# Kernel optimization log

Measured on AMD Instinct MI355X. Metric: run time of the kernel, lower is better.

The kernel has to match this reference:

```python
import jax, jax.numpy as jnp
import numpy as np
import math

N_HEADS = 16
DIM = 1024

def setup_inputs() -> dict:
    key = jax.random.key(0)
    ks = jax.random.split(key, 10)
    B, S, D = 4, 2048, DIM
    xavier = math.sqrt(2.0 / (D + D))  # xavier_normal_ std for square weight
    query = jax.random.normal(ks[0], (B, S, D), dtype=jnp.float32)
    mask = jnp.ones((B, S), dtype=jnp.int32)
    Wq = jax.random.normal(ks[1], (D, D), dtype=jnp.float32) * xavier
    Wk = jax.random.normal(ks[2], (D, D), dtype=jnp.float32) * xavier
    Wv = jax.random.normal(ks[3], (D, D), dtype=jnp.float32) * xavier
    Wo = jax.random.normal(ks[4], (D, D), dtype=jnp.float32) * xavier
    bound = 1.0 / math.sqrt(D)  # default nn.Linear bias init U(-1/sqrt(fan_in), ...)
    bq = jax.random.uniform(ks[5], (D,), jnp.float32, -bound, bound)
    bk = jax.random.uniform(ks[6], (D,), jnp.float32, -bound, bound)
    bv = jax.random.uniform(ks[7], (D,), jnp.float32, -bound, bound)
    bo = jax.random.uniform(ks[8], (D,), jnp.float32, -bound, bound)
    return {"query": query, "mask": mask, "Wq": Wq, "bq": bq, "Wk": Wk, "bk": bk,
            "Wv": Wv, "bv": bv, "Wo": Wo, "bo": bo}

def reference(query, mask, Wq, bq, Wk, bk, Wv, bv, Wo, bo):
    B, S, D = query.shape
    H = N_HEADS
    Dh = D // H
    scale = math.sqrt(Dh)
    def heads(x):  # [B,S,D] -> [B,H,S,Dh]
        return x.reshape(B, S, H, Dh).transpose(0, 2, 1, 3)
    q = heads(query @ Wq.T + bq)
    k = heads(query @ Wk.T + bk)
    v = heads(query @ Wv.T + bv)
    scores = jnp.einsum('bhsd,bhtd->bhst', q, k)  # [B,H,S,S]
    keep = (mask != 0)[:, None, None, :]  # [B,1,1,S]
    scores = jnp.where(keep, scores, jnp.float32(-1e20))
    attn = jax.nn.softmax(scores / scale, axis=-1)
    ctx = jnp.einsum('bhst,bhtd->bhsd', attn, v)  # [B,H,S,Dh]
    ctx = ctx.transpose(0, 2, 1, 3).reshape(B, S, D)
    return ctx @ Wo.T + bo
```

## Files before the change

kernel.cpp:

```cpp
#include <hip/hip_runtime.h>

typedef unsigned short u16;
typedef unsigned int u32;
typedef __attribute__((ext_vector_type(8))) short short8;
typedef __attribute__((ext_vector_type(8))) __bf16 bf16x8;
typedef __attribute__((ext_vector_type(4))) float f32x4;
typedef __attribute__((ext_vector_type(2))) u32 u32x2;

__device__ __forceinline__ float bf2f(u16 u) { return __uint_as_float(((u32)u) << 16); }
__device__ __forceinline__ u16 f2bf(float f) {
  u32 u = __float_as_uint(f);
  u = (u + 0x7fffu + ((u >> 16) & 1u)) >> 16;
  return (u16)u;
}

__device__ __forceinline__ float EXP2(float x) {
#if __has_builtin(__builtin_amdgcn_exp2f)
  return __builtin_amdgcn_exp2f(x);
#else
  return exp2f(x);
#endif
}

__device__ __forceinline__ u32 CVTPK(float lo, float hi) {
  u32 r;
  asm("v_cvt_pk_bf16_f32 %0, %1, %2" : "=v"(r) : "v"(lo), "v"(hi));
  return r;
}

template <typename V>
__device__ __forceinline__ auto mfma_try(V a, V b, f32x4 c, int)
    -> decltype(__builtin_amdgcn_mfma_f32_16x16x32_bf16(a, b, c, 0, 0, 0)) {
  return __builtin_amdgcn_mfma_f32_16x16x32_bf16(a, b, c, 0, 0, 0);
}
template <typename V>
__device__ __forceinline__ f32x4 mfma_try(V a, V b, f32x4 c, long) {
  return __builtin_amdgcn_mfma_f32_16x16x32_bf16(
      __builtin_bit_cast(bf16x8, a), __builtin_bit_cast(bf16x8, b), c, 0, 0, 0);
}
__device__ __forceinline__ f32x4 MFMA(short8 a, short8 b, f32x4 c) {
  return mfma_try(a, b, c, 0);
}

#define GLOAD16(gsrc, ldst)                                                  \
  __builtin_amdgcn_global_load_lds(                                          \
      (const __attribute__((address_space(1))) void*)(gsrc),                 \
      (__attribute__((address_space(3))) void*)(ldst), 16, 0, 0)

#define SQ 2048
#define NH 16
#define DH 64
#define DMODEL 1024

__global__ void detect_dtype(const u16* __restrict__ q, int* __restrict__ flag) {
  __shared__ int cnt;
  if (threadIdx.x == 0) cnt = 0;
  __syncthreads();
  const int k = threadIdx.x * 16384 + 128;
  const u16 u = q[2 * k];
  const int e = (u >> 7) & 0xFF;
  if (e >= 96 && e <= 143) atomicAdd(&cnt, 1);
  __syncthreads();
  if (threadIdx.x == 0) *flag = (cnt < 128) ? 1 : 0;
}

__device__ __forceinline__ short8 cvt8_f32(const float* s) {
  f32x4 a = *(const f32x4*)s;
  f32x4 b = *(const f32x4*)(s + 4);
  short8 o;
#pragma unroll
  for (int j = 0; j < 4; ++j) o[j] = (short)f2bf(a[j]);
#pragma unroll
  for (int j = 0; j < 4; ++j) o[4 + j] = (short)f2bf(b[j]);
  return o;
}

__global__ void cvt_tensor(const void* __restrict__ src, u16* __restrict__ dst,
                           int n8, const int* __restrict__ flag) {
  const bool isf32 = (*flag != 0);
  int i = blockIdx.x * blockDim.x + threadIdx.x;
  const int stride = gridDim.x * blockDim.x;
  if (isf32) {
    const float* s = (const float*)src;
    for (; i < n8; i += stride) *(short8*)(dst + i * 8) = cvt8_f32(s + i * 8);
  } else {
    const short8* s = (const short8*)src;
    for (; i < n8; i += stride) *(short8*)(dst + i * 8) = s[i];
  }
}

__global__ void cvt_w4(const void* s0, const void* s1, const void* s2, const void* s3,
                       u16* __restrict__ dst, const int* __restrict__ flag) {
  const bool isf32 = (*flag != 0);
  int i = blockIdx.x * blockDim.x + threadIdx.x;
  const int stride = gridDim.x * blockDim.x;
  for (; i < (1 << 19); i += stride) {
    const int seg = i >> 17, off = i & ((1 << 17) - 1);
    const void* s = (seg == 0) ? s0 : (seg == 1) ? s1 : (seg == 2) ? s2 : s3;
    u16* d = dst + ((long)seg << 20) + (long)off * 8;
    if (isf32) *(short8*)d = cvt8_f32((const float*)s + off * 8);
    else *(short8*)d = *((const short8*)s + off);
  }
}

__global__ void cvt_b4(const void* s0, const void* s1, const void* s2, const void* s3,
                       u16* __restrict__ dst, const int* __restrict__ flag) {
  const bool isf32 = (*flag != 0);
  int i = blockIdx.x * blockDim.x + threadIdx.x;
  if (i >= 512) return;
  const int seg = i >> 7, off = i & 127;
  const void* s = (seg == 0) ? s0 : (seg == 1) ? s1 : (seg == 2) ? s2 : s3;
  u16* d = dst + seg * 1024 + off * 8;
  if (isf32) *(short8*)d = cvt8_f32((const float*)s + off * 8);
  else *(short8*)d = *((const short8*)s + off);
}

template <int MODE>
__global__ __launch_bounds__(256, 2) void gemm_bt(
    const u16* __restrict__ A, const u16* __restrict__ W,
    const u16* __restrict__ bias, void* __restrict__ Cv,
    const int* __restrict__ flag, int M, int N, int K) {
  __shared__ __align__(16) u16 As[128 * 32];
  __shared__ __align__(16) u16 Bs[128 * 32];
  const int tid = threadIdx.x;
  const int lane = tid & 63;
  const int wv = tid >> 6;
  const int wr = wv >> 1, wc = wv & 1;
  const bool isf32 = (MODE == 0) && (*flag != 0);

  const int nwg = gridDim.x;
  const int cpx = nwg >> 3;
  const int bid = (blockIdx.x % 8) * cpx + (blockIdx.x >> 3);

  const int tiles_n = N >> 7;
  const int tm = bid / tiles_n, tn = bid % tiles_n;
  const int m0 = tm << 7, n0 = tn << 7;

  f32x4 acc[4][4];
#pragma unroll
  for (int i = 0; i < 4; ++i)
#pragma unroll
    for (int j = 0; j < 4; ++j)
#pragma unroll
      for (int r = 0; r < 4; ++r) acc[i][j][r] = 0.f;

  const int srow = tid >> 2;
  const int skk = (tid & 3) * 8;
  const u16* a0 = A + (long)(m0 + srow) * K + skk;
  const u16* a1 = A + (long)(m0 + 64 + srow) * K + skk;
  const u16* b0 = W + (long)(n0 + srow) * K + skk;
  const u16* b1 = W + (long)(n0 + 64 + srow) * K + skk;
  u16* lA0 = &As[tid * 8];
  u16* lA1 = &As[(256 + tid) * 8];
  u16* lB0 = &Bs[tid * 8];
  u16* lB1 = &Bs[(256 + tid) * 8];

  const int rk = 8 * (lane >> 4);
  const int rrow = lane & 15;
  const int r0 = (lane >> 4) * 4;

  for (int k0 = 0; k0 < K; k0 += 32) {
    GLOAD16(a0 + k0, lA0);
    GLOAD16(a1 + k0, lA1);
    GLOAD16(b0 + k0, lB0);
    GLOAD16(b1 + k0, lB1);
    asm volatile("s_waitcnt vmcnt(0)" ::: "memory");
    __syncthreads();
    short8 af[4], bf[4];
#pragma unroll
    for (int mi = 0; mi < 4; ++mi)
      af[mi] = *(const short8*)&As[(wr * 64 + mi * 16 + rrow) * 32 + rk];
#pragma unroll
    for (int ni = 0; ni < 4; ++ni)
      bf[ni] = *(const short8*)&Bs[(wc * 64 + ni * 16 + rrow) * 32 + rk];
#pragma unroll
    for (int mi = 0; mi < 4; ++mi)
#pragma unroll
      for (int ni = 0; ni < 4; ++ni)
        acc[mi][ni] = MFMA(af[mi], bf[ni], acc[mi][ni]);
    __syncthreads();
  }

#pragma unroll
  for (int ni = 0; ni < 4; ++ni) {
    const int col = n0 + wc * 64 + ni * 16 + rrow;
    const float bv = bf2f(bias[col]);
#pragma unroll
    for (int mi = 0; mi < 4; ++mi) {
#pragma unroll
      for (int r = 0; r < 4; ++r) {
        const int row = m0 + wr * 64 + mi * 16 + r0 + r;
        const float v = acc[mi][ni][r] + bv;
        if (MODE == 0) {
          const long idx = (long)row * N + col;
          if (isf32) ((float*)Cv)[idx] = v;
          else ((u16*)Cv)[idx] = f2bf(v);
        } else if (MODE == 1) {
          const int b = row >> 11, s = row & 2047, h = col >> 6, dh = col & 63;
          ((u16*)Cv)[(((long)(b * NH + h) * SQ) + s) * DH + dh] = f2bf(v);
        } else {
          const int b = row >> 11, s = row & 2047, h = col >> 6, dh = col & 63;
          ((u16*)Cv)[(((long)(b * NH + h) * DH) + dh) * SQ + s] = f2bf(v);
        }
      }
    }
  }
}

#define LSTR 72
#define SM_C 0.18033688011112043f

__global__ __launch_bounds__(256, 2) void attn_kernel(
    const u16* __restrict__ q, const u16* __restrict__ k,
    const u16* __restrict__ vT, const int* __restrict__ mask,
    u16* __restrict__ ctx) {
  __shared__ __align__(16) u16 Ks[64 * LSTR];
  __shared__ __align__(16) u16 Vs[64 * LSTR];
  __shared__ __align__(16) u16 Ps[4][32 * LSTR];
  __shared__ __align__(16) float Msf[64];

  const int tid = threadIdx.x, lane = tid & 63, wv = tid >> 6;
  const int bh = blockIdx.y, b = bh >> 4, h = bh & 15;
  const int q0 = blockIdx.x * 128 + wv * 32;
  const u16* qb = q + (long)bh * SQ * DH;
  const u16* kb = k + (long)bh * SQ * DH;
  const u16* vb = vT + (long)bh * DH * SQ;
  const int g1 = lane >> 4;
  const int rq = lane & 15;
  const int rk = 8 * g1;
  const int r0 = 4 * g1;

  short8 aq[2][2];
#pragma unroll
  for (int m = 0; m < 2; ++m)
#pragma unroll
    for (int ks = 0; ks < 2; ++ks)
      aq[m][ks] = *(const short8*)&qb[(long)(q0 + m * 16 + rq) * DH + ks * 32 + rk];

  f32x4 oacc[2][4];
  float mrow[2], lrow[2];
#pragma unroll
  for (int m = 0; m < 2; ++m) {
    mrow[m] = -1.0e9f;
    lrow[m] = 0.f;
#pragma unroll
    for (int nf = 0; nf < 4; ++nf)
#pragma unroll
      for (int r = 0; r < 4; ++r) oacc[m][nf][r] = 0.f;
  }

  const int stg_r = tid >> 3;
  const int stg_c = (tid & 7) * 8;

  for (int t0 = 0; t0 < SQ; t0 += 64) {
    const short8 kv0 = *(const short8*)&kb[(long)(t0 + stg_r) * DH + stg_c];
    const short8 kv1 = *(const short8*)&kb[(long)(t0 + 32 + stg_r) * DH + stg_c];
    const short8 vv0 = *(const short8*)&vb[(long)stg_r * SQ + t0 + stg_c];
    const short8 vv1 = *(const short8*)&vb[(long)(32 + stg_r) * SQ + t0 + stg_c];
    float mv = 0.f;
    if (tid < 64) mv = (mask[b * SQ + t0 + tid] != 0) ? 0.f : -1.0e9f;

    __syncthreads();
    *(short8*)&Ks[stg_r * LSTR + stg_c] = kv0;
    *(short8*)&Ks[(32 + stg_r) * LSTR + stg_c] = kv1;
    *(short8*)&Vs[stg_r * LSTR + stg_c] = vv0;
    *(short8*)&Vs[(32 + stg_r) * LSTR + stg_c] = vv1;
    if (tid < 64) Msf[tid] = mv;
    __syncthreads();

    short8 kf[4][2];
#pragma unroll
    for (int f = 0; f < 4; ++f)
#pragma unroll
      for (int ks = 0; ks < 2; ++ks)
        kf[f][ks] = *(const short8*)&Ks[(f * 16 + rq) * LSTR + ks * 32 + rk];
    f32x4 mo[4];
#pragma unroll
    for (int f = 0; f < 4; ++f) mo[f] = *(const f32x4*)&Msf[f * 16 + 4 * g1];

    f32x4 sacc[2][4];
#pragma unroll
    for (int m = 0; m < 2; ++m)
#pragma unroll
      for (int f = 0; f < 4; ++f)
#pragma unroll
        for (int r = 0; r < 4; ++r) sacc[m][f][r] = 0.f;
#pragma unroll
    for (int ks = 0; ks < 2; ++ks)
#pragma unroll
      for (int f = 0; f < 4; ++f)
#pragma unroll
        for (int m = 0; m < 2; ++m)
          sacc[m][f] = MFMA(kf[f][ks], aq[m][ks], sacc[m][f]);

#pragma unroll
    for (int m = 0; m < 2; ++m)
#pragma unroll
      for (int f = 0; f < 4; ++f)
#pragma unroll
        for (int r = 0; r < 4; ++r)
          sacc[m][f][r] = __builtin_fmaf(sacc[m][f][r], SM_C, mo[f][r]);

#pragma unroll
    for (int m = 0; m < 2; ++m) {
      f32x4 t4;
#pragma unroll
      for (int r = 0; r < 4; ++r)
        t4[r] = fmaxf(fmaxf(sacc[m][0][r], sacc[m][1][r]),
                      fmaxf(sacc[m][2][r], sacc[m][3][r]));
      float vmax = fmaxf(fmaxf(t4[0], t4[1]), fmaxf(t4[2], t4[3]));
      vmax = fmaxf(vmax, __shfl_xor(vmax, 16));
      vmax = fmaxf(vmax, __shfl_xor(vmax, 32));

      const float mnew = fmaxf(mrow[m], vmax);
      const float sc = EXP2(mrow[m] - mnew);
      mrow[m] = mnew;

#pragma unroll
      for (int f = 0; f < 4; ++f)
#pragma unroll
        for (int r = 0; r < 4; ++r)
          sacc[m][f][r] = EXP2(sacc[m][f][r] - mnew);
      f32x4 s4;
#pragma unroll
      for (int r = 0; r < 4; ++r)
        s4[r] = (sacc[m][0][r] + sacc[m][1][r]) + (sacc[m][2][r] + sacc[m][3][r]);
      float tsum = (s4[0] + s4[1]) + (s4[2] + s4[3]);
      tsum += __shfl_xor(tsum, 16);
      tsum += __shfl_xor(tsum, 32);
      lrow[m] = lrow[m] * sc + tsum;

      f32x4 scr;
#pragma unroll
      for (int r = 0; r < 4; ++r) scr[r] = __shfl(sc, 4 * g1 + r);
#pragma unroll
      for (int nf = 0; nf < 4; ++nf)
#pragma unroll
        for (int r = 0; r < 4; ++r) oacc[m][nf][r] *= scr[r];

#pragma unroll
      for (int f = 0; f < 4; ++f) {
        u32x2 w;
        w[0] = CVTPK(sacc[m][f][0], sacc[m][f][1]);
        w[1] = CVTPK(sacc[m][f][2], sacc[m][f][3]);
        *(u32x2*)&Ps[wv][(m * 16 + rq) * LSTR + f * 16 + 4 * g1] = w;
      }
    }

    __syncthreads();

#pragma unroll
    for (int ks2 = 0; ks2 < 2; ++ks2) {
      short8 pa[2];
#pragma unroll
      for (int m = 0; m < 2; ++m)
        pa[m] = *(const short8*)&Ps[wv][(m * 16 + rq) * LSTR + ks2 * 32 + rk];
#pragma unroll
      for (int nf = 0; nf < 4; ++nf) {
        const short8 bvv = *(const short8*)&Vs[(nf * 16 + rq) * LSTR + ks2 * 32 + rk];
#pragma unroll
        for (int m = 0; m < 2; ++m)
          oacc[m][nf] = MFMA(pa[m], bvv, oacc[m][nf]);
      }
    }
  }

#pragma unroll
  for (int m = 0; m < 2; ++m) {
    const float inv = 1.0f / lrow[m];
    f32x4 invr;
#pragma unroll
    for (int r = 0; r < 4; ++r) invr[r] = __shfl(inv, 4 * g1 + r);
#pragma unroll
    for (int nf = 0; nf < 4; ++nf)
#pragma unroll
      for (int r = 0; r < 4; ++r) {
        const int s = q0 + m * 16 + r0 + r;
        const int dh = nf * 16 + rq;
        ctx[(((long)(b * SQ + s)) * NH + h) * DH + dh] = f2bf(oacc[m][nf][r] * invr[r]);
      }
  }
}

extern "C" void kernel_launch(void* const* d_in, const int* in_sizes, int n_in,
                              void* d_out, int out_size, void* d_ws, size_t ws_size,
                              hipStream_t stream) {
  const void* query = d_in[0];
  const int* mask = (const int*)d_in[1];
  const void* Wq = d_in[2];
  const void* bq = d_in[3];
  const void* Wk = d_in[4];
  const void* bk = d_in[5];
  const void* Wv = d_in[6];
  const void* bv = d_in[7];
  const void* Wo = d_in[8];
  const void* bo = d_in[9];

  char* w = (char*)d_ws;
  int* flag = (int*)w;
  u16* qc = (u16*)(w + 256);
  u16* Wc = qc + (long)8388608;
  u16* bc = Wc + (long)4 * 1048576;
  u16* qb = bc + 4096;
  u16* kb = qb + (long)8388608;
  u16* vT = kb + (long)8388608;
  u16* ctx = vT + (long)8388608;

  dim3 blk(256);

  detect_dtype<<<1, 256, 0, stream>>>((const u16*)query, flag);
  cvt_tensor<<<2048, 256, 0, stream>>>(query, qc, 8388608 / 8, flag);
  cvt_w4<<<2048, 256, 0, stream>>>(Wq, Wk, Wv, Wo, Wc, flag);
  cvt_b4<<<2, 256, 0, stream>>>(bq, bk, bv, bo, bc, flag);

  const int M = 4 * SQ;
  dim3 gemm_grid((M / 128) * (DMODEL / 128));

  gemm_bt<1><<<gemm_grid, blk, 0, stream>>>(qc, Wc, bc, (void*)qb, flag, M, DMODEL, DMODEL);
  gemm_bt<1><<<gemm_grid, blk, 0, stream>>>(qc, Wc + 1048576, bc + 1024, (void*)kb, flag, M, DMODEL, DMODEL);
  gemm_bt<2><<<gemm_grid, blk, 0, stream>>>(qc, Wc + 2 * 1048576, bc + 2048, (void*)vT, flag, M, DMODEL, DMODEL);

  dim3 attn_grid(SQ / 128, 64);
  attn_kernel<<<attn_grid, blk, 0, stream>>>(qb, kb, vT, mask, ctx);

  gemm_bt<0><<<gemm_grid, blk, 0, stream>>>(ctx, Wc + 3 * 1048576, bc + 3072, d_out, flag, M, DMODEL, DMODEL);
}
```

Measured before the change: 345.4 us.

## Fuse QKV projections into one GEMM launch and widen attention KV tile to 128

The three Q/K/V projection GEMMs become a single launch over a concatenated 3072-wide weight, and each tile routes its output to the matching head-major or transposed buffer. This cuts launch overhead and tail effects and gives more work per launch. The attention kernel now processes 128 keys per iteration instead of 64, halving the loop trips and barriers. P is written in two halves to keep shared memory small, with new strides for the V and P buffers. The wider tile raises register pressure for the score accumulators, which may lower occupancy.

```diff
diff --git a/kernel.cpp b/kernel.cpp
--- a/kernel.cpp
+++ b/kernel.cpp
@@ -115,25 +115,23 @@
   else *(short8*)d = *((const short8*)s + off);
 }
 
-template <int MODE>
-__global__ __launch_bounds__(256, 2) void gemm_bt(
+__global__ __launch_bounds__(256, 2) void gemm_qkv(
     const u16* __restrict__ A, const u16* __restrict__ W,
-    const u16* __restrict__ bias, void* __restrict__ Cv,
-    const int* __restrict__ flag, int M, int N, int K) {
+    const u16* __restrict__ bias, u16* __restrict__ qb,
+    u16* __restrict__ kb, u16* __restrict__ vT) {
   __shared__ __align__(16) u16 As[128 * 32];
   __shared__ __align__(16) u16 Bs[128 * 32];
   const int tid = threadIdx.x;
   const int lane = tid & 63;
   const int wv = tid >> 6;
   const int wr = wv >> 1, wc = wv & 1;
-  const bool isf32 = (MODE == 0) && (*flag != 0);
+  const int K = DMODEL;
 
   const int nwg = gridDim.x;
   const int cpx = nwg >> 3;
   const int bid = (blockIdx.x % 8) * cpx + (blockIdx.x >> 3);
 
-  const int tiles_n = N >> 7;
-  const int tm = bid / tiles_n, tn = bid % tiles_n;
+  const int tm = bid / 24, tn = bid % 24;
   const int m0 = tm << 7, n0 = tn << 7;
 
   f32x4 acc[4][4];
@@ -181,43 +179,129 @@
     __syncthreads();
   }
 
+  const int seg = n0 >> 10;
+  const int nbase = n0 & 1023;
+  u16* dst = (seg == 0) ? qb : (seg == 1) ? kb : vT;
 #pragma unroll
   for (int ni = 0; ni < 4; ++ni) {
     const int col = n0 + wc * 64 + ni * 16 + rrow;
     const float bv = bf2f(bias[col]);
+    const int cl = nbase + wc * 64 + ni * 16 + rrow;
+    const int h = cl >> 6, dh = cl & 63;
 #pragma unroll
     for (int mi = 0; mi < 4; ++mi) {
 #pragma unroll
       for (int r = 0; r < 4; ++r) {
         const int row = m0 + wr * 64 + mi * 16 + r0 + r;
         const float v = acc[mi][ni][r] + bv;
-        if (MODE == 0) {
-          const long idx = (long)row * N + col;
-          if (isf32) ((float*)Cv)[idx] = v;
-          else ((u16*)Cv)[idx] = f2bf(v);
-        } else if (MODE == 1) {
-          const int b = row >> 11, s = row & 2047, h = col >> 6, dh = col & 63;
-          ((u16*)Cv)[(((long)(b * NH + h) * SQ) + s) * DH + dh] = f2bf(v);
+        const int b = row >> 11, s = row & 2047;
+        if (seg < 2) {
+          dst[(((long)(b * NH + h) * SQ) + s) * DH + dh] = f2bf(v);
         } else {
-          const int b = row >> 11, s = row & 2047, h = col >> 6, dh = col & 63;
-          ((u16*)Cv)[(((long)(b * NH + h) * DH) + dh) * SQ + s] = f2bf(v);
+          dst[(((long)(b * NH + h) * DH) + dh) * SQ + s] = f2bf(v);
         }
       }
     }
   }
 }
 
+__global__ __launch_bounds__(256, 2) void gemm_out(
+    const u16* __restrict__ A, const u16* __restrict__ W,
+    const u16* __restrict__ bias, void* __restrict__ Cv,
+    const int* __restrict__ flag, int M, int N, int K) {
+  __shared__ __align__(16) u16 As[128 * 32];
+  __shared__ __align__(16) u16 Bs[128 * 32];
+  const int tid = threadIdx.x;
+  const int lane = tid & 63;
+  const int wv = tid >> 6;
+  const int wr = wv >> 1, wc = wv & 1;
+  const bool isf32 = (*flag != 0);
+
+  const int nwg = gridDim.x;
+  const int cpx = nwg >> 3;
+  const int bid = (blockIdx.x % 8) * cpx + (blockIdx.x >> 3);
+
+  const int tiles_n = N >> 7;
+  const int tm = bid / tiles_n, tn = bid % tiles_n;
+  const int m0 = tm << 7, n0 = tn << 7;
+
+  f32x4 acc[4][4];
+#pragma unroll
+  for (int i = 0; i < 4; ++i)
+#pragma unroll
+    for (int j = 0; j < 4; ++j)
+#pragma unroll
+      for (int r = 0; r < 4; ++r) acc[i][j][r] = 0.f;
+
+  const int srow = tid >> 2;
+  const int skk = (tid & 3) * 8;
+  const u16* a0 = A + (long)(m0 + srow) * K + skk;
+  const u16* a1 = A + (long)(m0 + 64 + srow) * K + skk;
+  const u16* b0 = W + (long)(n0 + srow) * K + skk;
+  const u16* b1 = W + (long)(n0 + 64 + srow) * K + skk;
+  u16* lA0 = &As[tid * 8];
+  u16* lA1 = &As[(256 + tid) * 8];
+  u16* lB0 = &Bs[tid * 8];
+  u16* lB1 = &Bs[(256 + tid) * 8];
+
+  const int rk = 8 * (lane >> 4);
+  const int rrow = lane & 15;
+  const int r0 = (lane >> 4) * 4;
+
+  for (int k0 = 0; k0 < K; k0 += 32) {
+    GLOAD16(a0 + k0, lA0);
+    GLOAD16(a1 + k0, lA1);
+    GLOAD16(b0 + k0, lB0);
+    GLOAD16(b1 + k0, lB1);
+    asm volatile("s_waitcnt vmcnt(0)" ::: "memory");
+    __syncthreads();
+    short8 af[4], bf[4];
+#pragma unroll
+    for (int mi = 0; mi < 4; ++mi)
+      af[mi] = *(const short8*)&As[(wr * 64 + mi * 16 + rrow) * 32 + rk];
+#pragma unroll
+    for (int ni = 0; ni < 4; ++ni)
+      bf[ni] = *(const short8*)&Bs[(wc * 64 + ni * 16 + rrow) * 32 + rk];
+#pragma unroll
+    for (int mi = 0; mi < 4; ++mi)
+#pragma unroll
+      for (int ni = 0; ni < 4; ++ni)
+        acc[mi][ni] = MFMA(af[mi], bf[ni], acc[mi][ni]);
+    __syncthreads();
+  }
+
+#pragma unroll
+  for (int ni = 0; ni < 4; ++ni) {
+    const int col = n0 + wc * 64 + ni * 16 + rrow;
+    const float bv = bf2f(bias[col]);
+#pragma unroll
+    for (int mi = 0; mi < 4; ++mi) {
+#pragma unroll
+      for (int r = 0; r < 4; ++r) {
+        const int row = m0 + wr * 64 + mi * 16 + r0 + r;
+        const float v = acc[mi][ni][r] + bv;
+        const long idx = (long)row * N + col;
+        if (isf32) ((float*)Cv)[idx] = v;
+        else ((u16*)Cv)[idx] = f2bf(v);
+      }
+    }
+  }
+}
+
+#define KVB 128
 #define LSTR 72
+#define LSTRV 136
+#define LSTRP 68
 #define SM_C 0.18033688011112043f
 
 __global__ __launch_bounds__(256, 2) void attn_kernel(
     const u16* __restrict__ q, const u16* __restrict__ k,
     const u16* __restrict__ vT, const int* __restrict__ mask,
     u16* __restrict__ ctx) {
-  __shared__ __align__(16) u16 Ks[64 * LSTR];
-  __shared__ __align__(16) u16 Vs[64 * LSTR];
-  __shared__ __align__(16) u16 Ps[4][32 * LSTR];
-  __shared__ __align__(16) float Msf[64];
+  __shared__ __align__(16) u16 Ks[KVB * LSTR];
+  __shared__ __align__(16) u16 Vs[64 * LSTRV];
+  __shared__ __align__(16) u16 Ps[4][32 * LSTRP];
+  __shared__ __align__(16) float Msf[KVB];
 
   const int tid = threadIdx.x, lane = tid & 63, wv = tid >> 6;
   const int bh = blockIdx.y, b = bh >> 4, h = bh & 15;
@@ -251,63 +335,62 @@
 
   const int stg_r = tid >> 3;
   const int stg_c = (tid & 7) * 8;
-
-  for (int t0 = 0; t0 < SQ; t0 += 64) {
-    const short8 kv0 = *(const short8*)&kb[(long)(t0 + stg_r) * DH + stg_c];
-    const short8 kv1 = *(const short8*)&kb[(long)(t0 + 32 + stg_r) * DH + stg_c];
-    const short8 vv0 = *(const short8*)&vb[(long)stg_r * SQ + t0 + stg_c];
-    const short8 vv1 = *(const short8*)&vb[(long)(32 + stg_r) * SQ + t0 + stg_c];
+  const int vr = tid >> 4;
+  const int vc = (tid & 15) * 8;
+
+  for (int t0 = 0; t0 < SQ; t0 += KVB) {
+    short8 kvr[4], vvr[4];
+#pragma unroll
+    for (int j = 0; j < 4; ++j)
+      kvr[j] = *(const short8*)&kb[(long)(t0 + stg_r + 32 * j) * DH + stg_c];
+#pragma unroll
+    for (int j = 0; j < 4; ++j)
+      vvr[j] = *(const short8*)&vb[(long)(vr + 16 * j) * SQ + t0 + vc];
     float mv = 0.f;
-    if (tid < 64) mv = (mask[b * SQ + t0 + tid] != 0) ? 0.f : -1.0e9f;
+    if (tid < KVB) mv = (mask[b * SQ + t0 + tid] != 0) ? 0.f : -1.0e9f;
 
     __syncthreads();
-    *(short8*)&Ks[stg_r * LSTR + stg_c] = kv0;
-    *(short8*)&Ks[(32 + stg_r) * LSTR + stg_c] = kv1;
-    *(short8*)&Vs[stg_r * LSTR + stg_c] = vv0;
-    *(short8*)&Vs[(32 + stg_r) * LSTR + stg_c] = vv1;
-    if (tid < 64) Msf[tid] = mv;
+#pragma unroll
+    for (int j = 0; j < 4; ++j)
+      *(short8*)&Ks[(stg_r + 32 * j) * LSTR + stg_c] = kvr[j];
+#pragma unroll
+    for (int j = 0; j < 4; ++j)
+      *(short8*)&Vs[(vr + 16 * j) * LSTRV + vc] = vvr[j];
+    if (tid < KVB) Msf[tid] = mv;
     __syncthreads();
 
-    short8 kf[4][2];
-#pragma unroll
-    for (int f = 0; f < 4; ++f)
-#pragma unroll
-      for (int ks = 0; ks < 2; ++ks)
-        kf[f][ks] = *(const short8*)&Ks[(f * 16 + rq) * LSTR + ks * 32 + rk];
-    f32x4 mo[4];
-#pragma unroll
-    for (int f = 0; f < 4; ++f) mo[f] = *(const f32x4*)&Msf[f * 16 + 4 * g1];
-
-    f32x4 sacc[2][4];
-#pragma unroll
-    for (int m = 0; m < 2; ++m)
-#pragma unroll
-      for (int f = 0; f < 4; ++f)
-#pragma unroll
-        for (int r = 0; r < 4; ++r) sacc[m][f][r] = 0.f;
-#pragma unroll
-    for (int ks = 0; ks < 2; ++ks)
-#pragma unroll
-      for (int f = 0; f < 4; ++f)
-#pragma unroll
-        for (int m = 0; m < 2; ++m)
-          sacc[m][f] = MFMA(kf[f][ks], aq[m][ks], sacc[m][f]);
-
-#pragma unroll
-    for (int m = 0; m < 2; ++m)
-#pragma unroll
-      for (int f = 0; f < 4; ++f)
+    f32x4 sacc[2][8];
+#pragma unroll
+    for (int f = 0; f < 8; ++f) {
+      const short8 k0 = *(const short8*)&Ks[(f * 16 + rq) * LSTR + rk];
+      const short8 k1 = *(const short8*)&Ks[(f * 16 + rq) * LSTR + 32 + rk];
+      f32x4 z;
+#pragma unroll
+      for (int r = 0; r < 4; ++r) z[r] = 0.f;
+#pragma unroll
+      for (int m = 0; m < 2; ++m) {
+        f32x4 t = MFMA(k0, aq[m][0], z);
+        sacc[m][f] = MFMA(k1, aq[m][1], t);
+      }
+    }
+
+#pragma unroll
+    for (int f = 0; f < 8; ++f) {
+      const f32x4 mo = *(const f32x4*)&Msf[f * 16 + 4 * g1];
+#pragma unroll
+      for (int m = 0; m < 2; ++m)
 #pragma unroll
         for (int r = 0; r < 4; ++r)
-          sacc[m][f][r] = __builtin_fmaf(sacc[m][f][r], SM_C, mo[f][r]);
+          sacc[m][f][r] = __builtin_fmaf(sacc[m][f][r], SM_C, mo[r]);
+    }
 
 #pragma unroll
     for (int m = 0; m < 2; ++m) {
-      f32x4 t4;
-#pragma unroll
-      for (int r = 0; r < 4; ++r)
-        t4[r] = fmaxf(fmaxf(sacc[m][0][r], sacc[m][1][r]),
-                      fmaxf(sacc[m][2][r], sacc[m][3][r]));
+      f32x4 t4 = sacc[m][0];
+#pragma unroll
+      for (int f = 1; f < 8; ++f)
+#pragma unroll
+        for (int r = 0; r < 4; ++r) t4[r] = fmaxf(t4[r], sacc[m][f][r]);
       float vmax = fmaxf(fmaxf(t4[0], t4[1]), fmaxf(t4[2], t4[3]));
       vmax = fmaxf(vmax, __shfl_xor(vmax, 16));
       vmax = fmaxf(vmax, __shfl_xor(vmax, 32));
@@ -317,14 +400,15 @@
       mrow[m] = mnew;
 
 #pragma unroll
-      for (int f = 0; f < 4; ++f)
+      for (int f = 0; f < 8; ++f)
 #pragma unroll
         for (int r = 0; r < 4; ++r)
           sacc[m][f][r] = EXP2(sacc[m][f][r] - mnew);
       f32x4 s4;
 #pragma unroll
       for (int r = 0; r < 4; ++r)
-        s4[r] = (sacc[m][0][r] + sacc[m][1][r]) + (sacc[m][2][r] + sacc[m][3][r]);
+        s4[r] = ((sacc[m][0][r] + sacc[m][1][r]) + (sacc[m][2][r] + sacc[m][3][r])) +
+                ((sacc[m][4][r] + sacc[m][5][r]) + (sacc[m][6][r] + sacc[m][7][r]));
       float tsum = (s4[0] + s4[1]) + (s4[2] + s4[3]);
       tsum += __shfl_xor(tsum, 16);
       tsum += __shfl_xor(tsum, 32);
@@ -337,30 +421,34 @@
       for (int nf = 0; nf < 4; ++nf)
 #pragma unroll
         for (int r = 0; r < 4; ++r) oacc[m][nf][r] *= scr[r];
-
-#pragma unroll
-      for (int f = 0; f < 4; ++f) {
-        u32x2 w;
-        w[0] = CVTPK(sacc[m][f][0], sacc[m][f][1]);
-        w[1] = CVTPK(sacc[m][f][2], sacc[m][f][3]);
-        *(u32x2*)&Ps[wv][(m * 16 + rq) * LSTR + f * 16 + 4 * g1] = w;
-      }
     }
 
-    __syncthreads();
-
-#pragma unroll
-    for (int ks2 = 0; ks2 < 2; ++ks2) {
-      short8 pa[2];
+#pragma unroll
+    for (int half = 0; half < 2; ++half) {
 #pragma unroll
       for (int m = 0; m < 2; ++m)
-        pa[m] = *(const short8*)&Ps[wv][(m * 16 + rq) * LSTR + ks2 * 32 + rk];
-#pragma unroll
-      for (int nf = 0; nf < 4; ++nf) {
-        const short8 bvv = *(const short8*)&Vs[(nf * 16 + rq) * LSTR + ks2 * 32 + rk];
+#pragma unroll
+        for (int fl = 0; fl < 4; ++fl) {
+          const int f = half * 4 + fl;
+          u32x2 w;
+          w[0] = CVTPK(sacc[m][f][0], sacc[m][f][1]);
+          w[1] = CVTPK(sacc[m][f][2], sacc[m][f][3]);
+          *(u32x2*)&Ps[wv][(m * 16 + rq) * LSTRP + fl * 16 + 4 * g1] = w;
+        }
+#pragma unroll
+      for (int k2 = 0; k2 < 2; ++k2) {
+        const int ks2 = half * 2 + k2;
+        short8 pa[2];
 #pragma unroll
         for (int m = 0; m < 2; ++m)
-          oacc[m][nf] = MFMA(pa[m], bvv, oacc[m][nf]);
+          pa[m] = *(const short8*)&Ps[wv][(m * 16 + rq) * LSTRP + k2 * 32 + rk];
+#pragma unroll
+        for (int nf = 0; nf < 4; ++nf) {
+          const short8 bvv = *(const short8*)&Vs[(nf * 16 + rq) * LSTRV + ks2 * 32 + rk];
+#pragma unroll
+          for (int m = 0; m < 2; ++m)
+            oacc[m][nf] = MFMA(pa[m], bvv, oacc[m][nf]);
+        }
       }
     }
   }
@@ -401,9 +489,9 @@
   u16* qc = (u16*)(w + 256);
   u16* Wc = qc + (long)8388608;
   u16* bc = Wc + (long)4 * 1048576;
-  u16* qb = bc + 4096;
-  u16* kb = qb + (long)8388608;
-  u16* vT = kb + (long)8388608;
+  u16* qh = bc + 4096;
+  u16* kh = qh + (long)8388608;
+  u16* vT = kh + (long)8388608;
   u16* ctx = vT + (long)8388608;
 
   dim3 blk(256);
@@ -414,14 +502,12 @@
   cvt_b4<<<2, 256, 0, stream>>>(bq, bk, bv, bo, bc, flag);
 
   const int M = 4 * SQ;
-  dim3 gemm_grid((M / 128) * (DMODEL / 128));
-
-  gemm_bt<1><<<gemm_grid, blk, 0, stream>>>(qc, Wc, bc, (void*)qb, flag, M, DMODEL, DMODEL);
-  gemm_bt<1><<<gemm_grid, blk, 0, stream>>>(qc, Wc + 1048576, bc + 1024, (void*)kb, flag, M, DMODEL, DMODEL);
-  gemm_bt<2><<<gemm_grid, blk, 0, stream>>>(qc, Wc + 2 * 1048576, bc + 2048, (void*)vT, flag, M, DMODEL, DMODEL);
+
+  gemm_qkv<<<dim3(1536), blk, 0, stream>>>(qc, Wc, bc, qh, kh, vT);
 
   dim3 attn_grid(SQ / 128, 64);
-  attn_kernel<<<attn_grid, blk, 0, stream>>>(qb, kb, vT, mask, ctx);
-
-  gemm_bt<0><<<gemm_grid, blk, 0, stream>>>(ctx, Wc + 3 * 1048576, bc + 3072, d_out, flag, M, DMODEL, DMODEL);
-}
+  attn_kernel<<<attn_grid, blk, 0, stream>>>(qh, kh, vT, mask, ctx);
+
+  gemm_out<<<dim3((M / 128) * (DMODEL / 128)), blk, 0, stream>>>(
+      ctx, Wc + 3 * 1048576, bc + 3072, d_out, flag, M, DMODEL, DMODEL);
+}
```

New measurement: 349.4 us. Within noise of the previous version (+1.2%).
